# Optimization experiments

Hardware: AMD Instinct MI355X
Metric: run time of the kernel (lower is better)

## Reference

```python
import jax, jax.numpy as jnp
import numpy as np

NH = 8          # num_heads (init kwarg)
NUM_GROUPS = 32
EPS = 1e-5


def setup_inputs() -> dict:
    key = jax.random.key(0)
    ks = jax.random.split(key, 4)
    B, C, H, W = 2, 512, 64, 64
    x = jax.random.normal(ks[0], (B, C, H, W), dtype=jnp.float32)
    qkv_w = jax.random.normal(ks[1], (3 * C, C), dtype=jnp.float32) * (1.0 / np.sqrt(C))
    proj_w = jax.random.normal(ks[2], (C, C), dtype=jnp.float32) * (1.0 / np.sqrt(C))
    proj_b = jax.random.normal(ks[3], (C,), dtype=jnp.float32) * 0.02
    gn_w = jnp.ones((C,), dtype=jnp.float32)
    gn_b = jnp.zeros((C,), dtype=jnp.float32)
    return {"x": x, "qkv_w": qkv_w, "proj_w": proj_w, "proj_b": proj_b,
            "gn_w": gn_w, "gn_b": gn_b}


def _group_norm(x, gamma, beta):
    B, C, H, W = x.shape
    xg = x.reshape(B, NUM_GROUPS, C // NUM_GROUPS, H, W)
    mean = xg.mean(axis=(2, 3, 4), keepdims=True)
    var = xg.var(axis=(2, 3, 4), keepdims=True)
    xg = (xg - mean) * jax.lax.rsqrt(var + EPS)
    x = xg.reshape(B, C, H, W)
    return x * gamma[None, :, None, None] + beta[None, :, None, None]


def reference(x, qkv_w, proj_w, proj_b, gn_w, gn_b):
    B, C, H, W = x.shape
    h = _group_norm(x, gn_w, gn_b)
    # 1x1 conv == channel matmul
    qkv = jnp.einsum('oc,bchw->bohw', qkv_w, h)  # [B, 3C, H, W]
    # faithful legacy reshape: per-head contiguous [q,k,v] blocks of 3*C//NH channels
    qkv = qkv.reshape(B * NH, 3 * C // NH, H * W)
    q, k, v = jnp.split(qkv, 3, axis=1)          # each [B*NH, C//NH, HW]
    scale = 1.0 / np.sqrt(np.sqrt(C // NH))
    attn = jnp.einsum('bci,bcj->bij', q * scale, k * scale)  # [B*NH, HW, HW]
    attn = jax.nn.softmax(attn, axis=-1)
    hout = jnp.einsum('bij,bcj->bci', attn, v)   # [B*NH, C//NH, HW]
    hout = hout.reshape(B, C, H, W)
    hout = jnp.einsum('oc,bchw->bohw', proj_w, hout) + proj_b[None, :, None, None]
    return x + hout
```

## Files before the change

### kernel.cpp

```cpp
#include <hip/hip_runtime.h>
#include <math.h>

typedef __attribute__((ext_vector_type(8))) short short8;
typedef __attribute__((ext_vector_type(4))) short short4v;
typedef __attribute__((ext_vector_type(4))) float floatx4;
typedef __attribute__((ext_vector_type(16))) float floatx16;

__device__ __forceinline__ unsigned short f2bf(float f) {
  union { float f; unsigned int u; } v; v.f = f;
  unsigned int r = v.u + 0x7fffu + ((v.u >> 16) & 1u);
  return (unsigned short)(r >> 16);
}

__device__ __forceinline__ float bf2f(unsigned short h) {
  union { unsigned int u; float f; } v; v.u = ((unsigned int)h) << 16;
  return v.f;
}

__device__ __forceinline__ unsigned int pack2(unsigned short a, unsigned short b) {
  return (unsigned int)a | ((unsigned int)b << 16);
}

__device__ __forceinline__ unsigned int rbits(float f) {
  union { float f; unsigned int u; } v; v.f = f;
  return v.u + 0x8000u;
}

__device__ __forceinline__ float fast_exp2(float x) {
#if __has_builtin(__builtin_amdgcn_exp2f)
  return __builtin_amdgcn_exp2f(x);
#else
  return exp2f(x);
#endif
}

__device__ __forceinline__ void async16(const unsigned short* gp, unsigned short* lp) {
  __builtin_amdgcn_global_load_lds(
      (__attribute__((address_space(1))) void*)(gp),
      (__attribute__((address_space(3))) void*)(lp), 16, 0, 0);
}

__global__ void setup_kernel(const float* __restrict__ x, float* __restrict__ stats,
                             const float* __restrict__ qkv_w, unsigned short* __restrict__ wqkv,
                             const float* __restrict__ proj_w, unsigned short* __restrict__ wproj) {
  if (blockIdx.x < 64) {
    int bg = blockIdx.x;
    const float4* p = (const float4*)(x + (size_t)bg * 65536);
    float s = 0.f, ss = 0.f;
    for (int i = threadIdx.x; i < 16384; i += 256) {
      float4 v = p[i];
      s  += v.x + v.y + v.z + v.w;
      ss += v.x*v.x + v.y*v.y + v.z*v.z + v.w*v.w;
    }
    #pragma unroll
    for (int off = 32; off >= 1; off >>= 1) {
      s  += __shfl_xor(s,  off, 64);
      ss += __shfl_xor(ss, off, 64);
    }
    __shared__ float red[2][4];
    int wv = threadIdx.x >> 6;
    if ((threadIdx.x & 63) == 0) { red[0][wv] = s; red[1][wv] = ss; }
    __syncthreads();
    if (threadIdx.x == 0) {
      s  = red[0][0] + red[0][1] + red[0][2] + red[0][3];
      ss = red[1][0] + red[1][1] + red[1][2] + red[1][3];
      float mean = s * (1.f/65536.f);
      float var  = ss * (1.f/65536.f) - mean*mean;
      stats[2*bg]   = mean;
      stats[2*bg+1] = rsqrtf(var + 1e-5f);
    }
  } else {
    int i = (blockIdx.x - 64) * 256 + threadIdx.x;
    const float* s; unsigned short* d;
    if (i < 196608) { s = qkv_w; d = wqkv; }
    else { i -= 196608; s = proj_w; d = wproj; }
    float4 vv = ((const float4*)s)[i];
    uint2 o;
    o.x = pack2(f2bf(vv.x), f2bf(vv.y));
    o.y = pack2(f2bf(vv.z), f2bf(vv.w));
    ((uint2*)d)[i] = o;
  }
}

__global__ void gn_apply_t(const float* __restrict__ x, const float* __restrict__ stats,
                           const float* __restrict__ gw, const float* __restrict__ gb,
                           unsigned short* __restrict__ h_t) {
  __shared__ __align__(16) unsigned short tile[64][72];
  const int b = blockIdx.z, c0 = blockIdx.y * 64, hw0 = blockIdx.x * 64;
  const int t = threadIdx.x;
  {
    const int cl = t >> 2;
    const int hs = (t & 3) * 16;
    const int c  = c0 + cl;
    const int g  = c >> 4;
    const float mean = stats[2*(b*32 + g)];
    const float rstd = stats[2*(b*32 + g) + 1];
    const float w  = gw[c] * rstd;
    const float bb = gb[c] - mean * w;
    const float4* src = (const float4*)(x + ((size_t)(b*512 + c))*4096 + hw0 + hs);
    #pragma unroll
    for (int i = 0; i < 4; i++) {
      float4 vv = src[i];
      unsigned short* d = &tile[cl][hs + i*4];
      d[0] = f2bf(vv.x*w + bb); d[1] = f2bf(vv.y*w + bb);
      d[2] = f2bf(vv.z*w + bb); d[3] = f2bf(vv.w*w + bb);
    }
  }
  __syncthreads();
  {
    const int hwl = t >> 2;
    const int cs  = (t & 3) * 16;
    uint4 w0, w1;
    w0.x = pack2(tile[cs+ 0][hwl], tile[cs+ 1][hwl]);
    w0.y = pack2(tile[cs+ 2][hwl], tile[cs+ 3][hwl]);
    w0.z = pack2(tile[cs+ 4][hwl], tile[cs+ 5][hwl]);
    w0.w = pack2(tile[cs+ 6][hwl], tile[cs+ 7][hwl]);
    w1.x = pack2(tile[cs+ 8][hwl], tile[cs+ 9][hwl]);
    w1.y = pack2(tile[cs+10][hwl], tile[cs+11][hwl]);
    w1.z = pack2(tile[cs+12][hwl], tile[cs+13][hwl]);
    w1.w = pack2(tile[cs+14][hwl], tile[cs+15][hwl]);
    unsigned short* dst = h_t + ((size_t)(b*4096 + hw0 + hwl))*512 + c0 + cs;
    *(uint4*)dst       = w0;
    *(uint4*)(dst + 8) = w1;
  }
}

__global__ __launch_bounds__(256, 3)
void qkv_gemm(const unsigned short* __restrict__ A,
              const unsigned short* __restrict__ Bt,
              unsigned short* __restrict__ q_t,
              unsigned short* __restrict__ k_t,
              unsigned short* __restrict__ v_) {
  __shared__ __align__(16) unsigned short As[128*32];
  __shared__ __align__(16) unsigned short Bs[128*32];
  const int b   = blockIdx.z;
  const int n0  = blockIdx.x * 128;
  const int o0  = blockIdx.y * 128;
  const int tid = threadIdx.x;
  const int wave = tid >> 6, lane = tid & 63;
  const int wr = wave >> 1, wc = wave & 1;
  const int fm = lane & 15, fq = lane >> 4;
  const int srow = lane >> 2, scol = (lane & 3) * 8;

  const unsigned short* Ab = A + (size_t)o0 * 512;
  const unsigned short* Bb = Bt + ((size_t)b*4096 + n0) * 512;

  bool vsw[4];
  #pragma unroll
  for (int fr = 0; fr < 4; fr++) {
    const int ob = o0 + wr*64 + fr*16;
    vsw[fr] = ((ob % 192) >> 6) == 2;
  }

  floatx4 acc[4][4];
  #pragma unroll
  for (int i = 0; i < 4; i++)
    #pragma unroll
    for (int j = 0; j < 4; j++) acc[i][j] = (floatx4){0.f,0.f,0.f,0.f};

  for (int k0 = 0; k0 < 512; k0 += 32) {
    __syncthreads();
    #pragma unroll
    for (int cc = 0; cc < 2; cc++) {
      int ch = wave*2 + cc;
      async16(Ab + (size_t)(ch*16 + srow)*512 + k0 + scol, &As[ch*512]);
      async16(Bb + (size_t)(ch*16 + srow)*512 + k0 + scol, &Bs[ch*512]);
    }
    __syncthreads();
    short8 af[4], bf[4];
    #pragma unroll
    for (int f = 0; f < 4; f++) {
      af[f] = *(const short8*)&As[(wr*64 + f*16 + fm)*32 + fq*8];
      bf[f] = *(const short8*)&Bs[(wc*64 + f*16 + fm)*32 + fq*8];
    }
    #pragma unroll
    for (int fr = 0; fr < 4; fr++) {
      if (vsw[fr]) {
        #pragma unroll
        for (int fc = 0; fc < 4; fc++)
          acc[fr][fc] = __builtin_amdgcn_mfma_f32_16x16x32_bf16(bf[fc], af[fr], acc[fr][fc], 0, 0, 0);
      } else {
        #pragma unroll
        for (int fc = 0; fc < 4; fc++)
          acc[fr][fc] = __builtin_amdgcn_mfma_f32_16x16x32_bf16(af[fr], bf[fc], acc[fr][fc], 0, 0, 0);
      }
    }
  }

  #pragma unroll
  for (int fr = 0; fr < 4; fr++) {
    const int ob     = o0 + wr*64 + fr*16;
    const int head   = ob / 192;
    const int rem    = ob % 192;
    const int region = rem >> 6;
    const int bhh    = b*8 + head;
    #pragma unroll
    for (int fc = 0; fc < 4; fc++) {
      if (region == 0) {
        const int i = n0 + wc*64 + fc*16 + fm;
        const int dsub = (rem & 63) + fq*4;
        unsigned short t4[4];
        #pragma unroll
        for (int r = 0; r < 4; r++) t4[r] = f2bf(acc[fr][fc][r] * 0.18033688f);
        uint2 o; o.x = pack2(t4[0], t4[1]); o.y = pack2(t4[2], t4[3]);
        *(uint2*)&q_t[((size_t)bhh*4096 + i)*64 + dsub] = o;
      } else if (region == 1) {
        const int i = n0 + wc*64 + fc*16 + fm;
        const int dsub = (rem & 63) + fq*4;
        unsigned short t4[4];
        #pragma unroll
        for (int r = 0; r < 4; r++) t4[r] = f2bf(acc[fr][fc][r]);
        uint2 o; o.x = pack2(t4[0], t4[1]); o.y = pack2(t4[2], t4[3]);
        *(uint2*)&k_t[((size_t)bhh*4096 + i)*64 + dsub] = o;
      } else {
        const int dsub = (rem & 63) + fm;
        const int tok0 = n0 + wc*64 + fc*16 + fq*4;
        unsigned short t4[4];
        #pragma unroll
        for (int r = 0; r < 4; r++) t4[r] = f2bf(acc[fr][fc][r]);
        uint2 o; o.x = pack2(t4[0], t4[1]); o.y = pack2(t4[2], t4[3]);
        *(uint2*)&v_[((size_t)bhh*64 + dsub)*4096 + tok0] = o;
      }
    }
  }
}

__global__ __launch_bounds__(256, 2)
void proj_gemm(const unsigned short* __restrict__ A,
               const unsigned short* __restrict__ Bt,
               float* __restrict__ outp,
               const float* __restrict__ xres,
               const float* __restrict__ pbias) {
  __shared__ __align__(16) unsigned short As[64*32];
  __shared__ __align__(16) unsigned short Bs[128*32];
  const int b   = blockIdx.z;
  const int n0  = blockIdx.x * 128;
  const int o0  = blockIdx.y * 64;
  const int tid = threadIdx.x;
  const int wave = tid >> 6, lane = tid & 63;
  const int wr = wave >> 1, wc = wave & 1;
  const int fm = lane & 15, fq = lane >> 4;
  const int srow = lane >> 2, scol = (lane & 3) * 8;

  const unsigned short* Ab = A + (size_t)o0 * 512;
  const unsigned short* Bb = Bt + ((size_t)b*4096 + n0) * 512;

  floatx4 acc[2][4];
  #pragma unroll
  for (int i = 0; i < 2; i++)
    #pragma unroll
    for (int j = 0; j < 4; j++) acc[i][j] = (floatx4){0.f,0.f,0.f,0.f};

  for (int k0 = 0; k0 < 512; k0 += 32) {
    __syncthreads();
    async16(Ab + (size_t)(wave*16 + srow)*512 + k0 + scol, &As[wave*512]);
    #pragma unroll
    for (int cc = 0; cc < 2; cc++) {
      int ch = wave*2 + cc;
      async16(Bb + (size_t)(ch*16 + srow)*512 + k0 + scol, &Bs[ch*512]);
    }
    __syncthreads();
    short8 af[2], bf[4];
    #pragma unroll
    for (int f = 0; f < 2; f++)
      af[f] = *(const short8*)&As[(wr*32 + f*16 + fm)*32 + fq*8];
    #pragma unroll
    for (int f = 0; f < 4; f++)
      bf[f] = *(const short8*)&Bs[(wc*64 + f*16 + fm)*32 + fq*8];
    #pragma unroll
    for (int fr = 0; fr < 2; fr++)
      #pragma unroll
      for (int fc = 0; fc < 4; fc++)
        acc[fr][fc] = __builtin_amdgcn_mfma_f32_16x16x32_bf16(af[fr], bf[fc], acc[fr][fc], 0, 0, 0);
  }

  #pragma unroll
  for (int fr = 0; fr < 2; fr++)
    #pragma unroll
    for (int fc = 0; fc < 4; fc++) {
      const int i = n0 + wc*64 + fc*16 + fm;
      #pragma unroll
      for (int r = 0; r < 4; r++) {
        const int o = o0 + wr*32 + fr*16 + fq*4 + r;
        const size_t idx = ((size_t)b*512 + o)*4096 + i;
        outp[idx] = xres[idx] + pbias[o] + acc[fr][fc][r];
      }
    }
}

template <int SPLIT>
__global__ __launch_bounds__(256, 2)
void attn_kernel(const unsigned short* __restrict__ q_t,
                 const unsigned short* __restrict__ k_t,
                 const unsigned short* __restrict__ v_,
                 unsigned short* __restrict__ hout_t,
                 unsigned short* __restrict__ o_part,
                 float* __restrict__ l_part) {
  __shared__ __align__(16) unsigned short Ks[2][64*72];
  __shared__ __align__(16) unsigned short Vs[2][64*72];

  const int bh  = blockIdx.x;
  const int q0  = blockIdx.y * 256;
  const int js  = SPLIT ? blockIdx.z : 0;
  const int nit = SPLIT ? 32 : 64;
  const int jbase = js * 2048;
  const int tid = threadIdx.x;
  const int wave = tid >> 6, lane = tid & 63;
  const int ln = lane & 31, h = lane >> 5;

  short8 qf[2][4];
  #pragma unroll
  for (int ih = 0; ih < 2; ih++) {
    const unsigned short* qrow = q_t + ((size_t)bh*4096 + q0 + wave*64 + ih*32 + ln)*64;
    #pragma unroll
    for (int kc = 0; kc < 4; kc++)
      qf[ih][kc] = *(const short8*)(qrow + kc*16 + h*8);
  }

  const floatx16 z16 = {0.f,0.f,0.f,0.f,0.f,0.f,0.f,0.f,
                        0.f,0.f,0.f,0.f,0.f,0.f,0.f,0.f};
  floatx16 o_acc[2][2];
  #pragma unroll
  for (int ih = 0; ih < 2; ih++) { o_acc[ih][0] = z16; o_acc[ih][1] = z16; }
  float l0 = 0.f, l1 = 0.f;

  const int sr = tid >> 3;
  const int sc = (tid & 7) * 8;
  const int cch = tid & 7;
  const int vpos = ((cch >> 2) * 32) + ((cch & 3) * 4);
  const unsigned short* kbase = k_t + (size_t)bh*262144;
  const unsigned short* vbase = v_  + (size_t)bh*262144;

  uint4 kr0 = *(const uint4*)&kbase[(size_t)(jbase + sr)*64 + sc];
  uint4 kr1 = *(const uint4*)&kbase[(size_t)(jbase + sr + 32)*64 + sc];
  uint4 vr0 = *(const uint4*)&vbase[(size_t)sr*4096 + jbase + sc];
  uint4 vr1 = *(const uint4*)&vbase[(size_t)(sr+32)*4096 + jbase + sc];

  for (int it = 0; it < nit; it++) {
    unsigned short* Kc = Ks[it & 1];
    unsigned short* Vc = Vs[it & 1];
    *(uint4*)&Kc[sr*72 + sc]      = kr0;
    *(uint4*)&Kc[(sr+32)*72 + sc] = kr1;
    *(uint2*)&Vc[sr*72 + vpos]           = *(const uint2*)&vr0;
    *(uint2*)&Vc[sr*72 + vpos + 16]      = *((const uint2*)&vr0 + 1);
    *(uint2*)&Vc[(sr+32)*72 + vpos]      = *(const uint2*)&vr1;
    *(uint2*)&Vc[(sr+32)*72 + vpos + 16] = *((const uint2*)&vr1 + 1);
    __syncthreads();

    {
      const int jn = jbase + (((it + 1) & (nit - 1)) * 64);
      kr0 = *(const uint4*)&kbase[(size_t)(jn + sr)*64 + sc];
      kr1 = *(const uint4*)&kbase[(size_t)(jn + sr + 32)*64 + sc];
      vr0 = *(const uint4*)&vbase[(size_t)sr*4096 + jn + sc];
      vr1 = *(const uint4*)&vbase[(size_t)(sr+32)*4096 + jn + sc];
    }

    #pragma unroll
    for (int mj = 0; mj < 2; mj++) {
      short8 kf[4];
      #pragma unroll
      for (int kc = 0; kc < 4; kc++)
        kf[kc] = *(const short8*)&Kc[(mj*32 + ln)*72 + kc*16 + h*8];
      short8 vv[2][2];
      #pragma unroll
      for (int dn = 0; dn < 2; dn++)
        #pragma unroll
        for (int t2 = 0; t2 < 2; t2++)
          vv[dn][t2] = *(const short8*)&Vc[(dn*32 + ln)*72 + mj*32 + h*16 + t2*8];

      #pragma unroll
      for (int ih = 0; ih < 2; ih++) {
        floatx16 st = __builtin_amdgcn_mfma_f32_32x32x16_bf16(kf[0], qf[ih][0], z16, 0, 0, 0);
        #pragma unroll
        for (int kc = 1; kc < 4; kc++)
          st = __builtin_amdgcn_mfma_f32_32x32x16_bf16(kf[kc], qf[ih][kc], st, 0, 0, 0);

        unsigned pk[8];
        float lacc = 0.f;
        #pragma unroll
        for (int rp = 0; rp < 8; rp++) {
          float p0 = fast_exp2(st[2*rp]);
          float p1 = fast_exp2(st[2*rp + 1]);
          lacc += p0 + p1;
          pk[rp] = __builtin_amdgcn_perm(rbits(p1), rbits(p0), 0x07060302u);
        }
        if (ih) l1 += lacc; else l0 += lacc;

        #pragma unroll
        for (int t2 = 0; t2 < 2; t2++) {
          union { unsigned u[2]; short4v s; } a0, a1;
          a0.u[0] = pk[4*t2];     a0.u[1] = pk[4*t2 + 1];
          a1.u[0] = pk[4*t2 + 2]; a1.u[1] = pk[4*t2 + 3];
          #pragma unroll
          for (int dn = 0; dn < 2; dn++) {
            short4v vlo = __builtin_shufflevector(vv[dn][t2], vv[dn][t2], 0, 1, 2, 3);
            short4v vhi = __builtin_shufflevector(vv[dn][t2], vv[dn][t2], 4, 5, 6, 7);
            o_acc[ih][dn] = __builtin_amdgcn_mfma_f32_32x32x8bf16_1k(a0.s, vlo, o_acc[ih][dn], 0, 0, 0);
            o_acc[ih][dn] = __builtin_amdgcn_mfma_f32_32x32x8bf16_1k(a1.s, vhi, o_acc[ih][dn], 0, 0, 0);
          }
        }
      }
    }
  }

  l0 += __shfl_xor(l0, 32, 64);
  l1 += __shfl_xor(l1, 32, 64);

  if (SPLIT) {
    #pragma unroll
    for (int ih = 0; ih < 2; ih++) {
      unsigned short* op = o_part +
          (((size_t)(js*16 + bh)*4096 + q0 + wave*64 + ih*32) * 64);
      #pragma unroll
      for (int r = 0; r < 16; r++) {
        const int il = (r & 3) + 8*(r >> 2) + 4*h;
        op[(size_t)il*64 + ln]      = f2bf(o_acc[ih][0][r]);
        op[(size_t)il*64 + 32 + ln] = f2bf(o_acc[ih][1][r]);
      }
    }
    if (lane < 32) {
      l_part[(size_t)(js*16 + bh)*4096 + q0 + wave*64 + lane]      = l0;
      l_part[(size_t)(js*16 + bh)*4096 + q0 + wave*64 + 32 + lane] = l1;
    }
  } else {
    const float linv0 = 1.f / l0;
    const float linv1 = 1.f / l1;
    const int bb = bh >> 3;
    const int cb = (bh & 7) * 64;
    #pragma unroll
    for (int ih = 0; ih < 2; ih++) {
      #pragma unroll
      for (int r = 0; r < 16; r++) {
        const int il = (r & 3) + 8*(r >> 2) + 4*h;
        const float inv = __shfl(ih ? linv1 : linv0, il, 64);
        const int i = q0 + wave*64 + ih*32 + il;
        unsigned short* dst = &hout_t[((size_t)bb*4096 + i)*512 + cb + ln];
        dst[0]  = f2bf(o_acc[ih][0][r] * inv);
        dst[32] = f2bf(o_acc[ih][1][r] * inv);
      }
    }
  }
}

__global__ void attn_combine(const unsigned short* __restrict__ o_part,
                             const float* __restrict__ l_part,
                             unsigned short* __restrict__ hout_t) {
  const int bh = blockIdx.x;
  const int i0 = blockIdx.y * 64;
  const int t  = threadIdx.x;
  const int d4 = (t & 15) * 4;
  const int il = t >> 4;
  const int bb = bh >> 3;
  const int cb = (bh & 7) * 64;
  const size_t JS = (size_t)16 * 4096 * 64;
  #pragma unroll
  for (int p = 0; p < 4; p++) {
    const int i = i0 + p*16 + il;
    const size_t ob = ((size_t)bh*4096 + i)*64 + d4;
    uint2 a = *(const uint2*)&o_part[ob];
    uint2 b = *(const uint2*)&o_part[ob + JS];
    const size_t lb = (size_t)bh*4096 + i;
    const float inv = 1.f / (l_part[lb] + l_part[lb + 65536]);
    float o0 = (bf2f((unsigned short)(a.x & 0xffff)) + bf2f((unsigned short)(b.x & 0xffff))) * inv;
    float o1 = (bf2f((unsigned short)(a.x >> 16))    + bf2f((unsigned short)(b.x >> 16)))    * inv;
    float o2 = (bf2f((unsigned short)(a.y & 0xffff)) + bf2f((unsigned short)(b.y & 0xffff))) * inv;
    float o3 = (bf2f((unsigned short)(a.y >> 16))    + bf2f((unsigned short)(b.y >> 16)))    * inv;
    uint2 w;
    w.x = pack2(f2bf(o0), f2bf(o1));
    w.y = pack2(f2bf(o2), f2bf(o3));
    *(uint2*)&hout_t[((size_t)bb*4096 + i)*512 + cb + d4] = w;
  }
}

extern "C" void kernel_launch(void* const* d_in, const int* in_sizes, int n_in,
                              void* d_out, int out_size, void* d_ws, size_t ws_size,
                              hipStream_t stream) {
  (void)in_sizes; (void)n_in; (void)out_size;
  const float* x      = (const float*)d_in[0];
  const float* qkv_w  = (const float*)d_in[1];
  const float* proj_w = (const float*)d_in[2];
  const float* proj_b = (const float*)d_in[3];
  const float* gn_w   = (const float*)d_in[4];
  const float* gn_b   = (const float*)d_in[5];
  float* out = (float*)d_out;

  char* ws = (char*)d_ws;
  unsigned short* h_t   = (unsigned short*)(ws);
  unsigned short* q_t   = (unsigned short*)(ws + ((size_t)8  << 20));
  unsigned short* k_t   = (unsigned short*)(ws + ((size_t)16 << 20));
  unsigned short* v_    = (unsigned short*)(ws + ((size_t)24 << 20));
  unsigned short* wqkv  = (unsigned short*)(ws + ((size_t)32 << 20));
  unsigned short* wproj = (unsigned short*)(ws + ((size_t)34 << 20));
  float* stats          = (float*)(ws + ((size_t)35 << 20));
  unsigned short* o_part = (unsigned short*)(ws + ((size_t)36 << 20));
  float* l_part          = (float*)(ws + ((size_t)52 << 20));
  unsigned short* hout_t = h_t;

  const bool split = ws_size >= (((size_t)52 << 20) + ((size_t)1 << 19));

  setup_kernel<<<dim3(1088), dim3(256), 0, stream>>>(x, stats, qkv_w, wqkv, proj_w, wproj);
  gn_apply_t<<<dim3(64, 8, 2), dim3(256), 0, stream>>>(x, stats, gn_w, gn_b, h_t);
  qkv_gemm<<<dim3(32, 12, 2), dim3(256), 0, stream>>>(wqkv, h_t, q_t, k_t, v_);
  if (split) {
    attn_kernel<1><<<dim3(16, 16, 2), dim3(256), 0, stream>>>(q_t, k_t, v_, nullptr,
                                                              o_part, l_part);
    attn_combine<<<dim3(16, 64), dim3(256), 0, stream>>>(o_part, l_part, hout_t);
  } else {
    attn_kernel<0><<<dim3(16, 16), dim3(256), 0, stream>>>(q_t, k_t, v_, hout_t,
                                                           nullptr, nullptr);
  }
  proj_gemm<<<dim3(32, 8, 2), dim3(256), 0, stream>>>(wproj, hout_t, out, x, proj_b);
}
```

Baseline: 221.3 us.

## Generalize attention KV split to up to four partitions and raise occupancy

The attention kernel now splits the key/value range into up to four partitions, chosen from the available workspace size. The combine kernel sums a variable number of partial outputs and row sums. Launch bounds move from 2 to 4 blocks per SM to allow more occupancy, and s_setprio hints wrap the MFMA sections so they can overlap with other waves' exp work. The extra partials add write and read traffic in the combine step, and the tighter register budget may cause spills.

```diff
diff --git a/kernel.cpp b/kernel.cpp
--- a/kernel.cpp
+++ b/kernel.cpp
@@ -288,8 +288,8 @@
     }
 }
 
-template <int SPLIT>
-__global__ __launch_bounds__(256, 2)
+template <int NSPLIT>
+__global__ __launch_bounds__(256, 4)
 void attn_kernel(const unsigned short* __restrict__ q_t,
                  const unsigned short* __restrict__ k_t,
                  const unsigned short* __restrict__ v_,
@@ -301,9 +301,11 @@
 
   const int bh  = blockIdx.x;
   const int q0  = blockIdx.y * 256;
-  const int js  = SPLIT ? blockIdx.z : 0;
-  const int nit = SPLIT ? 32 : 64;
-  const int jbase = js * 2048;
+  const int js  = (NSPLIT > 1) ? blockIdx.z : 0;
+  const int t0  = (js * 64) / NSPLIT;
+  const int t1  = ((js + 1) * 64) / NSPLIT;
+  const int nt  = t1 - t0;
+  const int jbase = t0 * 64;
   const int tid = threadIdx.x;
   const int wave = tid >> 6, lane = tid & 63;
   const int ln = lane & 31, h = lane >> 5;
@@ -336,7 +338,7 @@
   uint4 vr0 = *(const uint4*)&vbase[(size_t)sr*4096 + jbase + sc];
   uint4 vr1 = *(const uint4*)&vbase[(size_t)(sr+32)*4096 + jbase + sc];
 
-  for (int it = 0; it < nit; it++) {
+  for (int it = 0; it < nt; it++) {
     unsigned short* Kc = Ks[it & 1];
     unsigned short* Vc = Vs[it & 1];
     *(uint4*)&Kc[sr*72 + sc]      = kr0;
@@ -348,7 +350,8 @@
     __syncthreads();
 
     {
-      const int jn = jbase + (((it + 1) & (nit - 1)) * 64);
+      int itn = it + 1; if (itn == nt) itn = 0;
+      const int jn = (t0 + itn) * 64;
       kr0 = *(const uint4*)&kbase[(size_t)(jn + sr)*64 + sc];
       kr1 = *(const uint4*)&kbase[(size_t)(jn + sr + 32)*64 + sc];
       vr0 = *(const uint4*)&vbase[(size_t)sr*4096 + jn + sc];
@@ -370,22 +373,25 @@
 
       #pragma unroll
       for (int ih = 0; ih < 2; ih++) {
+        __builtin_amdgcn_s_setprio(1);
         floatx16 st = __builtin_amdgcn_mfma_f32_32x32x16_bf16(kf[0], qf[ih][0], z16, 0, 0, 0);
         #pragma unroll
         for (int kc = 1; kc < 4; kc++)
           st = __builtin_amdgcn_mfma_f32_32x32x16_bf16(kf[kc], qf[ih][kc], st, 0, 0, 0);
+        __builtin_amdgcn_s_setprio(0);
 
         unsigned pk[8];
-        float lacc = 0.f;
+        float la = 0.f, lb = 0.f;
         #pragma unroll
         for (int rp = 0; rp < 8; rp++) {
           float p0 = fast_exp2(st[2*rp]);
           float p1 = fast_exp2(st[2*rp + 1]);
-          lacc += p0 + p1;
+          la += p0; lb += p1;
           pk[rp] = __builtin_amdgcn_perm(rbits(p1), rbits(p0), 0x07060302u);
         }
-        if (ih) l1 += lacc; else l0 += lacc;
-
+        if (ih) l1 += la + lb; else l0 += la + lb;
+
+        __builtin_amdgcn_s_setprio(1);
         #pragma unroll
         for (int t2 = 0; t2 < 2; t2++) {
           union { unsigned u[2]; short4v s; } a0, a1;
@@ -399,6 +405,7 @@
             o_acc[ih][dn] = __builtin_amdgcn_mfma_f32_32x32x8bf16_1k(a1.s, vhi, o_acc[ih][dn], 0, 0, 0);
           }
         }
+        __builtin_amdgcn_s_setprio(0);
       }
     }
   }
@@ -406,7 +413,7 @@
   l0 += __shfl_xor(l0, 32, 64);
   l1 += __shfl_xor(l1, 32, 64);
 
-  if (SPLIT) {
+  if (NSPLIT > 1) {
     #pragma unroll
     for (int ih = 0; ih < 2; ih++) {
       unsigned short* op = o_part +
@@ -444,7 +451,8 @@
 
 __global__ void attn_combine(const unsigned short* __restrict__ o_part,
                              const float* __restrict__ l_part,
-                             unsigned short* __restrict__ hout_t) {
+                             unsigned short* __restrict__ hout_t,
+                             int nsplit) {
   const int bh = blockIdx.x;
   const int i0 = blockIdx.y * 64;
   const int t  = threadIdx.x;
@@ -453,21 +461,24 @@
   const int bb = bh >> 3;
   const int cb = (bh & 7) * 64;
   const size_t JS = (size_t)16 * 4096 * 64;
+  const size_t LS = (size_t)16 * 4096;
   #pragma unroll
   for (int p = 0; p < 4; p++) {
     const int i = i0 + p*16 + il;
-    const size_t ob = ((size_t)bh*4096 + i)*64 + d4;
-    uint2 a = *(const uint2*)&o_part[ob];
-    uint2 b = *(const uint2*)&o_part[ob + JS];
-    const size_t lb = (size_t)bh*4096 + i;
-    const float inv = 1.f / (l_part[lb] + l_part[lb + 65536]);
-    float o0 = (bf2f((unsigned short)(a.x & 0xffff)) + bf2f((unsigned short)(b.x & 0xffff))) * inv;
-    float o1 = (bf2f((unsigned short)(a.x >> 16))    + bf2f((unsigned short)(b.x >> 16)))    * inv;
-    float o2 = (bf2f((unsigned short)(a.y & 0xffff)) + bf2f((unsigned short)(b.y & 0xffff))) * inv;
-    float o3 = (bf2f((unsigned short)(a.y >> 16))    + bf2f((unsigned short)(b.y >> 16)))    * inv;
+    float o0 = 0.f, o1 = 0.f, o2 = 0.f, o3 = 0.f, l = 0.f;
+    for (int ns = 0; ns < nsplit; ns++) {
+      const size_t ob = ((size_t)bh*4096 + i)*64 + d4 + (size_t)ns*JS;
+      uint2 a = *(const uint2*)&o_part[ob];
+      o0 += bf2f((unsigned short)(a.x & 0xffff));
+      o1 += bf2f((unsigned short)(a.x >> 16));
+      o2 += bf2f((unsigned short)(a.y & 0xffff));
+      o3 += bf2f((unsigned short)(a.y >> 16));
+      l  += l_part[(size_t)bh*4096 + i + (size_t)ns*LS];
+    }
+    const float inv = 1.f / l;
     uint2 w;
-    w.x = pack2(f2bf(o0), f2bf(o1));
-    w.y = pack2(f2bf(o2), f2bf(o3));
+    w.x = pack2(f2bf(o0 * inv), f2bf(o1 * inv));
+    w.y = pack2(f2bf(o2 * inv), f2bf(o3 * inv));
     *(uint2*)&hout_t[((size_t)bb*4096 + i)*512 + cb + d4] = w;
   }
 }
@@ -492,22 +503,41 @@
   unsigned short* wqkv  = (unsigned short*)(ws + ((size_t)32 << 20));
   unsigned short* wproj = (unsigned short*)(ws + ((size_t)34 << 20));
   float* stats          = (float*)(ws + ((size_t)35 << 20));
-  unsigned short* o_part = (unsigned short*)(ws + ((size_t)36 << 20));
-  float* l_part          = (float*)(ws + ((size_t)52 << 20));
   unsigned short* hout_t = h_t;
 
-  const bool split = ws_size >= (((size_t)52 << 20) + ((size_t)1 << 19));
+  const size_t base      = (size_t)36 << 20;
+  const size_t opart_per = (size_t)8 << 20;
+  const size_t lpart_per = (size_t)1 << 18;
+  int nsplit = 1;
+  if      (ws_size >= base + 4*(opart_per + lpart_per)) nsplit = 4;
+  else if (ws_size >= base + 3*(opart_per + lpart_per)) nsplit = 3;
+  else if (ws_size >= base + 2*(opart_per + lpart_per)) nsplit = 2;
+
+  unsigned short* o_part = (unsigned short*)(ws + base);
+  float* l_part          = (float*)(ws + base + (size_t)nsplit * opart_per);
 
   setup_kernel<<<dim3(1088), dim3(256), 0, stream>>>(x, stats, qkv_w, wqkv, proj_w, wproj);
   gn_apply_t<<<dim3(64, 8, 2), dim3(256), 0, stream>>>(x, stats, gn_w, gn_b, h_t);
   qkv_gemm<<<dim3(32, 12, 2), dim3(256), 0, stream>>>(wqkv, h_t, q_t, k_t, v_);
-  if (split) {
-    attn_kernel<1><<<dim3(16, 16, 2), dim3(256), 0, stream>>>(q_t, k_t, v_, nullptr,
-                                                              o_part, l_part);
-    attn_combine<<<dim3(16, 64), dim3(256), 0, stream>>>(o_part, l_part, hout_t);
-  } else {
-    attn_kernel<0><<<dim3(16, 16), dim3(256), 0, stream>>>(q_t, k_t, v_, hout_t,
-                                                           nullptr, nullptr);
-  }
+  switch (nsplit) {
+    case 4:
+      attn_kernel<4><<<dim3(16, 16, 4), dim3(256), 0, stream>>>(q_t, k_t, v_, nullptr,
+                                                                o_part, l_part);
+      break;
+    case 3:
+      attn_kernel<3><<<dim3(16, 16, 3), dim3(256), 0, stream>>>(q_t, k_t, v_, nullptr,
+                                                                o_part, l_part);
+      break;
+    case 2:
+      attn_kernel<2><<<dim3(16, 16, 2), dim3(256), 0, stream>>>(q_t, k_t, v_, nullptr,
+                                                                o_part, l_part);
+      break;
+    default:
+      attn_kernel<1><<<dim3(16, 16), dim3(256), 0, stream>>>(q_t, k_t, v_, hout_t,
+                                                             nullptr, nullptr);
+      break;
+  }
+  if (nsplit > 1)
+    attn_combine<<<dim3(16, 64), dim3(256), 0, stream>>>(o_part, l_part, hout_t, nsplit);
   proj_gemm<<<dim3(32, 8, 2), dim3(256), 0, stream>>>(wproj, hout_t, out, x, proj_b);
 }
```

Result: slower. 872.1 us (+294.2%).
